# Performance work log

Hardware: AMD Instinct MI355X
Metric: run time of the kernel (lower is better)

Reference implementation:

```python
import jax, jax.numpy as jnp
import numpy as np

B, P, K_NB, D, H = 4, 1024, 32, 768, 12
S = P + 1
HD = D // H  # 64

def _ln(x, w, b):
    m = jnp.mean(x, -1, keepdims=True)
    v = jnp.var(x, -1, keepdims=True)
    return (x - m) / jnp.sqrt(v + 1e-5) * w + b

def setup_inputs() -> dict:
    key = jax.random.key(0)
    ks = jax.random.split(key, 8)
    w = lambda k, sh: jax.random.normal(k, sh, jnp.float32) * 0.02
    return {
        'x': jax.random.normal(ks[0], (B, S, D), jnp.float32),
        'routes': jax.random.randint(ks[1], (P, K_NB), 0, P, dtype=jnp.int32),
        'qkv_w': w(ks[2], (D, 3 * D)), 'qkv_b': jnp.zeros((3 * D,), jnp.float32),
        'proj_w': w(ks[3], (D, D)), 'proj_b': jnp.zeros((D,), jnp.float32),
        'ln1_w': jnp.ones((D,), jnp.float32), 'ln1_b': jnp.zeros((D,), jnp.float32),
        'ln2_w': jnp.ones((D,), jnp.float32), 'ln2_b': jnp.zeros((D,), jnp.float32),
        'mlp_w1': w(ks[4], (D, 4 * D)), 'mlp_b1': jnp.zeros((4 * D,), jnp.float32),
        'mlp_w2': w(ks[5], (4 * D, D)), 'mlp_b2': jnp.zeros((D,), jnp.float32),
    }

def reference(x, routes, qkv_w, qkv_b, proj_w, proj_b, ln1_w, ln1_b,
              ln2_w, ln2_b, mlp_w1, mlp_b1, mlp_w2, mlp_b2):
    scale = HD ** -0.5
    xn = _ln(x, ln1_w, ln1_b)
    qkv = (xn @ qkv_w + qkv_b).reshape(B, S, 3, H, HD).transpose(2, 0, 3, 1, 4)
    Q, Kt, V = qkv[0], qkv[1], qkv[2]  # each [B,H,S,HD]
    # CLS token: full dense attention over all S tokens
    sc = jnp.einsum('bhqd,bhkd->bhqk', Q[:, :, :1], Kt) * scale
    oc = jnp.einsum('bhqk,bhkd->bhqd', jax.nn.softmax(sc, -1), V)  # [B,H,1,HD]
    # patch tokens: sparse attention over k routed neighbors
    r = routes + 1  # shift past CLS (buffer routes_shifted)
    Kg = Kt[:, :, r, :]  # [B,H,P,k,HD] gathered keys
    Vg = V[:, :, r, :]   # [B,H,P,k,HD] gathered values
    sp = jnp.einsum('bhpd,bhpkd->bhpk', Q[:, :, 1:], Kg) * scale
    op = jnp.einsum('bhpk,bhpkd->bhpd', jax.nn.softmax(sp, -1), Vg)
    out = jnp.concatenate([oc, op], axis=2).transpose(0, 2, 1, 3).reshape(B, S, D)
    x = x + (out @ proj_w + proj_b)
    h = _ln(x, ln2_w, ln2_b)
    h = jax.nn.gelu(h @ mlp_w1 + mlp_b1, approximate=False) @ mlp_w2 + mlp_b2
    return x + h
```

## Files before the change

kernel.cpp:

```cpp
#include <hip/hip_runtime.h>
#include <hip/hip_bf16.h>

using bf16 = __hip_bfloat16;
using s8v  = __attribute__((ext_vector_type(8))) short;
using f4v  = __attribute__((ext_vector_type(4))) float;

constexpr int B_   = 4;
constexpr int P_   = 1024;
constexpr int KNB  = 32;
constexpr int D_   = 768;
constexpr int H_   = 12;
constexpr int S_   = P_ + 1;
constexpr int M_   = B_ * S_;
constexpr int MPAD = 4224;

#define DEVI static __device__ __forceinline__
#define WAITVM(N) asm volatile("s_waitcnt vmcnt(" #N ")" ::: "memory")
#define MEMFENCE  asm volatile("" ::: "memory")

DEVI float b2f_lo(unsigned u) { return __builtin_bit_cast(float, u << 16); }
DEVI float b2f_hi(unsigned u) { return __builtin_bit_cast(float, u & 0xffff0000u); }
DEVI float bu2f(unsigned short u) { return __builtin_bit_cast(float, (unsigned)u << 16); }
DEVI unsigned short f2bu(float f) {
  return __builtin_bit_cast(unsigned short, __float2bfloat16(f));
}

template<int KK, int NN>
__global__ __launch_bounds__(256)
void wt_conv(const float* __restrict__ W, bf16* __restrict__ Wt) {
  __shared__ float t[32][33];
  int bk = blockIdx.x * 32, bn = blockIdx.y * 32;
  int tx = threadIdx.x & 31, ty = threadIdx.x >> 5;
#pragma unroll
  for (int i = 0; i < 32; i += 8)
    t[ty + i][tx] = W[(size_t)(bk + ty + i) * NN + bn + tx];
  __syncthreads();
#pragma unroll
  for (int i = 0; i < 32; i += 8)
    Wt[(size_t)(bn + ty + i) * KK + bk + tx] = __float2bfloat16(t[tx][ty + i]);
}

__global__ __launch_bounds__(256)
void ln_kernel(const float* __restrict__ x, const float* __restrict__ w,
               const float* __restrict__ b, bf16* __restrict__ out) {
  int row = blockIdx.x;
  const float* xr = x + (size_t)row * D_;
  int t = threadIdx.x;
  float v0 = xr[t], v1 = xr[t + 256], v2 = xr[t + 512];
  float s = v0 + v1 + v2;
  float ss = v0 * v0 + v1 * v1 + v2 * v2;
#pragma unroll
  for (int o = 32; o; o >>= 1) { s += __shfl_xor(s, o); ss += __shfl_xor(ss, o); }
  __shared__ float sm[4], sv[4];
  if ((t & 63) == 0) { sm[t >> 6] = s; sv[t >> 6] = ss; }
  __syncthreads();
  float S = sm[0] + sm[1] + sm[2] + sm[3];
  float SS = sv[0] + sv[1] + sv[2] + sv[3];
  float mean = S * (1.f / D_);
  float var  = SS * (1.f / D_) - mean * mean;
  float inv  = rsqrtf(var + 1e-5f);
  bf16* orow = out + (size_t)row * D_;
  orow[t]       = __float2bfloat16((v0 - mean) * inv * w[t]       + b[t]);
  orow[t + 256] = __float2bfloat16((v1 - mean) * inv * w[t + 256] + b[t + 256]);
  orow[t + 512] = __float2bfloat16((v2 - mean) * inv * w[t + 512] + b[t + 512]);
}

template<int BM, int N, int KSTRIDE, int KCHUNK, int MODE>
__global__ __launch_bounds__(256)
void gemm_bf16(const bf16* __restrict__ A, const bf16* __restrict__ Bt,
               const float* __restrict__ bias, void* __restrict__ dst) {
  constexpr int MR   = BM / 32;
  constexpr int LPS  = BM / 64 + 2;
  constexpr int TN   = N / 128;
  constexpr int NBLK = (MPAD / BM) * TN;
  __shared__ bf16 ldsA[3][BM * 32];
  __shared__ bf16 ldsB[3][128 * 32];

  int bid = blockIdx.x;
  constexpr int NQ = NBLK >> 3, NR = NBLK & 7;
  int xcd = bid & 7, off = bid >> 3;
  int swz = (xcd < NR ? xcd * (NQ + 1) : NR * (NQ + 1) + (xcd - NR) * NQ) + off;
  const int tm = swz / TN, tn = swz % TN;
  const int kbase = blockIdx.y * KCHUNK;

  const int tid = threadIdx.x;
  const int wid = tid >> 6, lane = tid & 63;
  const int wr = wid >> 1, wc = wid & 1;

  auto stage = [&](int bufi, int step) {
    const int k0 = kbase + step * 32;
#pragma unroll
    for (int i = 0; i < BM / 64; ++i) {
      int c = wid * 64 + i * 256 + lane;
      int r = c >> 2, slot = c & 3;
      int gs = slot ^ ((r >> 1) & 3);
      const bf16* ga = A + (size_t)(tm * BM + r) * KSTRIDE + k0 + gs * 8;
      bf16* la = &ldsA[bufi][(wid * 64 + i * 256) * 8];
      __builtin_amdgcn_global_load_lds(
          (__attribute__((address_space(1))) void*)ga,
          (__attribute__((address_space(3))) void*)la, 16, 0, 0);
    }
#pragma unroll
    for (int i = 0; i < 2; ++i) {
      int c = wid * 64 + i * 256 + lane;
      int r = c >> 2, slot = c & 3;
      int gs = slot ^ ((r >> 1) & 3);
      const bf16* ga = Bt + (size_t)(tn * 128 + r) * KSTRIDE + k0 + gs * 8;
      bf16* la = &ldsB[bufi][(wid * 64 + i * 256) * 8];
      __builtin_amdgcn_global_load_lds(
          (__attribute__((address_space(1))) void*)ga,
          (__attribute__((address_space(3))) void*)la, 16, 0, 0);
    }
  };

  f4v acc[MR][4] = {};
  const int nk = KCHUNK / 32;

  stage(0, 0); stage(1, 1);

#pragma unroll 3
  for (int kt = 0; kt < nk; ++kt) {
    if (kt < nk - 1) {
      if constexpr (LPS == 4) WAITVM(4); else WAITVM(3);
    } else {
      WAITVM(0);
    }
    __builtin_amdgcn_s_barrier();
    MEMFENCE;
    if (kt + 2 < nk) stage((kt + 2) % 3, kt + 2);

    const int cur = kt % 3;
    s8v af[MR], bfv[4];
#pragma unroll
    for (int m = 0; m < MR; ++m) {
      int row = wr * (MR * 16) + m * 16 + (lane & 15);
      int slot = (lane >> 4) ^ ((row >> 1) & 3);
      af[m] = *(const s8v*)&ldsA[cur][row * 32 + slot * 8];
    }
#pragma unroll
    for (int n = 0; n < 4; ++n) {
      int row = wc * 64 + n * 16 + (lane & 15);
      int slot = (lane >> 4) ^ ((row >> 1) & 3);
      bfv[n] = *(const s8v*)&ldsB[cur][row * 32 + slot * 8];
    }
    __builtin_amdgcn_s_setprio(1);
#pragma unroll
    for (int m = 0; m < MR; ++m)
#pragma unroll
      for (int n = 0; n < 4; ++n)
        acc[m][n] = __builtin_amdgcn_mfma_f32_16x16x32_bf16(af[m], bfv[n], acc[m][n], 0, 0, 0);
    __builtin_amdgcn_s_setprio(0);
  }

#pragma unroll
  for (int m = 0; m < MR; ++m)
#pragma unroll
    for (int n = 0; n < 4; ++n)
#pragma unroll
      for (int j = 0; j < 4; ++j) {
        int row = tm * BM + wr * (MR * 16) + m * 16 + (lane >> 4) * 4 + j;
        int col = tn * 128 + wc * 64 + n * 16 + (lane & 15);
        float v = acc[m][n][j];
        if (MODE == 0) {
          if (row < M_) {
            float val = v + bias[col];
            int which = col / 768, rem2 = col % 768;
            int bb = row / S_, s = row % S_;
            ((bf16*)dst)[((size_t)(which * B_ + bb) * S_ + s) * 768 + rem2] =
                __float2bfloat16(val);
          }
        } else if (MODE == 2) {
          if (row < M_) {
            float val = v + bias[col];
            val = 0.5f * val * (1.f + erff(val * 0.70710678f));
            ((bf16*)dst)[(size_t)row * N + col] = __float2bfloat16(val);
          }
        } else {
          bf16* p = (bf16*)dst + (size_t)blockIdx.y * MPAD * N;
          p[(size_t)row * N + col] = __float2bfloat16(v);
        }
      }
}

template<bool IP>
__global__ __launch_bounds__(256)
void reduceK(const bf16* __restrict__ part, const float* __restrict__ src,
             const float* __restrict__ bias, float* __restrict__ out) {
  int i = blockIdx.x * 256 + threadIdx.x;
  ushort4 a = ((const ushort4*)part)[i];
  ushort4 b = ((const ushort4*)(part + (size_t)MPAD * 768))[i];
  float4 s = IP ? ((const float4*)out)[i] : ((const float4*)src)[i];
  int col = (i * 4) % D_;
  float4 bv = *(const float4*)&bias[col];
  float4 o;
  o.x = s.x + bv.x + bu2f(a.x) + bu2f(b.x);
  o.y = s.y + bv.y + bu2f(a.y) + bu2f(b.y);
  o.z = s.z + bv.z + bu2f(a.z) + bu2f(b.z);
  o.w = s.w + bv.w + bu2f(a.w) + bu2f(b.w);
  ((float4*)out)[i] = o;
}

__global__ __launch_bounds__(256)
void cls_partial(const bf16* __restrict__ QKV, float* __restrict__ part) {
  int bh = blockIdx.x, c = blockIdx.y;
  int b = bh / H_, h = bh % H_;
  const bf16* q  = QKV + ((size_t)(0 * B_ + b) * S_) * D_ + h * 64;
  const bf16* Kr = QKV + ((size_t)(1 * B_ + b) * S_) * D_ + h * 64;
  const bf16* Vr = QKV + ((size_t)(2 * B_ + b) * S_) * D_ + h * 64;
  int k0 = c * 256, kn = (c == 3) ? 257 : 256;
  __shared__ float qf[64];
  __shared__ float sc[257];
  __shared__ float red[4];
  __shared__ float pv[4][64];
  int t = threadIdx.x;
  if (t < 64) qf[t] = __bfloat162float(q[t]);
  __syncthreads();
  for (int kk = t; kk < kn; kk += 256) {
    const uint4* k4 = (const uint4*)(Kr + (size_t)(k0 + kk) * D_);
    float s = 0.f;
#pragma unroll
    for (int i = 0; i < 8; ++i) {
      uint4 kv = k4[i];
      const float* q8 = &qf[i * 8];
      s += b2f_lo(kv.x) * q8[0] + b2f_hi(kv.x) * q8[1]
         + b2f_lo(kv.y) * q8[2] + b2f_hi(kv.y) * q8[3]
         + b2f_lo(kv.z) * q8[4] + b2f_hi(kv.z) * q8[5]
         + b2f_lo(kv.w) * q8[6] + b2f_hi(kv.w) * q8[7];
    }
    sc[kk] = s * 0.125f;
  }
  __syncthreads();
  float mx = -1e30f;
  for (int kk = t; kk < kn; kk += 256) mx = fmaxf(mx, sc[kk]);
#pragma unroll
  for (int o = 32; o; o >>= 1) mx = fmaxf(mx, __shfl_xor(mx, o));
  if ((t & 63) == 0) red[t >> 6] = mx;
  __syncthreads();
  float M = fmaxf(fmaxf(red[0], red[1]), fmaxf(red[2], red[3]));
  __syncthreads();
  float sum = 0.f;
  for (int kk = t; kk < kn; kk += 256) { float e = __expf(sc[kk] - M); sc[kk] = e; sum += e; }
#pragma unroll
  for (int o = 32; o; o >>= 1) sum += __shfl_xor(sum, o);
  if ((t & 63) == 0) red[t >> 6] = sum;
  __syncthreads();
  float L = red[0] + red[1] + red[2] + red[3];
  int d = t & 63, kg = t >> 6;
  float acc = 0.f;
  for (int kk = kg; kk < kn; kk += 4)
    acc += sc[kk] * __bfloat162float(Vr[(size_t)(k0 + kk) * D_ + d]);
  pv[kg][d] = acc;
  __syncthreads();
  float* pp = part + ((size_t)bh * 4 + c) * 68;
  if (t < 64) pp[4 + t] = pv[0][t] + pv[1][t] + pv[2][t] + pv[3][t];
  else if (t == 64) pp[0] = M;
  else if (t == 65) pp[1] = L;
}

__global__ __launch_bounds__(64)
void cls_combine(const float* __restrict__ part, bf16* __restrict__ out) {
  int bh = blockIdx.x, t = threadIdx.x;
  const float* pp = part + (size_t)bh * 4 * 68;
  float m0 = pp[0], m1 = pp[68], m2 = pp[136], m3 = pp[204];
  float M = fmaxf(fmaxf(m0, m1), fmaxf(m2, m3));
  float e0 = __expf(m0 - M), e1 = __expf(m1 - M), e2 = __expf(m2 - M), e3 = __expf(m3 - M);
  float L = pp[1] * e0 + pp[69] * e1 + pp[137] * e2 + pp[205] * e3;
  float o = pp[4 + t] * e0 + pp[72 + t] * e1 + pp[140 + t] * e2 + pp[208 + t] * e3;
  int b = bh / H_, h = bh % H_;
  out[(size_t)(b * S_) * D_ + h * 64 + t] = __float2bfloat16(o / L);
}

__global__ __launch_bounds__(256)
void routed_attn(const bf16* __restrict__ QKV, const int* __restrict__ routes,
                 bf16* __restrict__ out) {
  int unit = blockIdx.x * 4 + (threadIdx.x >> 6);
  int lane = threadIdx.x & 63;
  int h = unit % H_;
  int bp = unit / H_;
  int p = bp % P_, b = bp / P_;

  int k = lane & 31, hi = lane >> 5;
  int r = routes[p * KNB + k] + 1;

  const bf16* Qp = QKV + ((size_t)(0 * B_ + b) * S_ + (p + 1)) * D_ + h * 64 + hi * 32;
  const bf16* Kb = QKV + ((size_t)(1 * B_ + b) * S_) * D_;
  const bf16* Vb = QKV + ((size_t)(2 * B_ + b) * S_) * D_;

  const uint4* q4 = (const uint4*)Qp;
  const uint4* k4 = (const uint4*)(Kb + (size_t)r * D_ + h * 64 + hi * 32);
  float dot = 0.f;
#pragma unroll
  for (int i = 0; i < 4; ++i) {
    uint4 qv = q4[i], kv = k4[i];
    dot += b2f_lo(kv.x) * b2f_lo(qv.x) + b2f_hi(kv.x) * b2f_hi(qv.x)
         + b2f_lo(kv.y) * b2f_lo(qv.y) + b2f_hi(kv.y) * b2f_hi(qv.y)
         + b2f_lo(kv.z) * b2f_lo(qv.z) + b2f_hi(kv.z) * b2f_hi(qv.z)
         + b2f_lo(kv.w) * b2f_lo(qv.w) + b2f_hi(kv.w) * b2f_hi(qv.w);
  }
  dot += __shfl_xor(dot, 32);
  float sc = dot * 0.125f;

  float mx = sc;
#pragma unroll
  for (int o = 16; o; o >>= 1) mx = fmaxf(mx, __shfl_xor(mx, o));
  float w = __expf(sc - mx);
  float sum = w;
#pragma unroll
  for (int o = 16; o; o >>= 1) sum += __shfl_xor(sum, o);
  float inv = 1.f / sum;

  int c = lane & 7, kr0 = lane >> 3;
  float acc[8] = {};
#pragma unroll
  for (int j = 0; j < 4; ++j) {
    int kj = (kr0 & 7) + 8 * j;
    float wj = __shfl(w, kj);
    int rj = __shfl(r, kj);
    uint4 vv = *(const uint4*)(Vb + (size_t)rj * D_ + h * 64 + c * 8);
    acc[0] += wj * b2f_lo(vv.x); acc[1] += wj * b2f_hi(vv.x);
    acc[2] += wj * b2f_lo(vv.y); acc[3] += wj * b2f_hi(vv.y);
    acc[4] += wj * b2f_lo(vv.z); acc[5] += wj * b2f_hi(vv.z);
    acc[6] += wj * b2f_lo(vv.w); acc[7] += wj * b2f_hi(vv.w);
  }
#pragma unroll
  for (int s = 8; s < 64; s <<= 1)
#pragma unroll
    for (int d = 0; d < 8; ++d) acc[d] += __shfl_xor(acc[d], s);

  if (lane < 8) {
    s8v o;
#pragma unroll
    for (int d = 0; d < 8; ++d) o[d] = (short)f2bu(acc[d] * inv);
    *(s8v*)(out + ((size_t)(b * S_ + p + 1)) * D_ + h * 64 + c * 8) = o;
  }
}

extern "C" void kernel_launch(void* const* d_in, const int* in_sizes, int n_in,
                              void* d_out, int out_size, void* d_ws, size_t ws_size,
                              hipStream_t stream) {
  const float* x      = (const float*)d_in[0];
  const int*   routes = (const int*)d_in[1];
  const float* qkv_w  = (const float*)d_in[2];
  const float* qkv_b  = (const float*)d_in[3];
  const float* proj_w = (const float*)d_in[4];
  const float* proj_b = (const float*)d_in[5];
  const float* ln1_w  = (const float*)d_in[6];
  const float* ln1_b  = (const float*)d_in[7];
  const float* ln2_w  = (const float*)d_in[8];
  const float* ln2_b  = (const float*)d_in[9];
  const float* mlp_w1 = (const float*)d_in[10];
  const float* mlp_b1 = (const float*)d_in[11];
  const float* mlp_w2 = (const float*)d_in[12];
  const float* mlp_b2 = (const float*)d_in[13];
  float* out = (float*)d_out;

  bf16* qkvw_t  = (bf16*)d_ws;
  bf16* projw_t = qkvw_t + 2304 * 768;
  bf16* mlpw1_t = projw_t + 768 * 768;
  bf16* mlpw2_t = mlpw1_t + 3072 * 768;
  bf16* xnA     = mlpw2_t + 768 * 3072;
  bf16* qkvbuf  = xnA + (size_t)MPAD * 768;
  bf16* attn    = qkvbuf + (size_t)3 * B_ * S_ * 768;
  bf16* h2      = attn + (size_t)MPAD * 768;
  bf16* g       = xnA;
  bf16* projp   = xnA;
  bf16* mlp2p   = attn;
  float* clsp   = (float*)(attn + (size_t)M_ * 768);

  wt_conv<768, 2304><<<dim3(24, 72), 256, 0, stream>>>(qkv_w, qkvw_t);
  wt_conv<768, 768><<<dim3(24, 24), 256, 0, stream>>>(proj_w, projw_t);
  wt_conv<768, 3072><<<dim3(24, 96), 256, 0, stream>>>(mlp_w1, mlpw1_t);
  wt_conv<3072, 768><<<dim3(96, 24), 256, 0, stream>>>(mlp_w2, mlpw2_t);

  ln_kernel<<<M_, 256, 0, stream>>>(x, ln1_w, ln1_b, xnA);

  gemm_bf16<128, 2304, 768, 768, 0><<<33 * 18, 256, 0, stream>>>(xnA, qkvw_t, qkv_b, qkvbuf);

  routed_attn<<<(B_ * P_ * H_) / 4, 256, 0, stream>>>(qkvbuf, routes, attn);
  cls_partial<<<dim3(B_ * H_, 4), 256, 0, stream>>>(qkvbuf, clsp);
  cls_combine<<<B_ * H_, 64, 0, stream>>>(clsp, attn);

  gemm_bf16<64, 768, 768, 384, 3><<<dim3(66 * 6, 2), 256, 0, stream>>>(attn, projw_t, nullptr, projp);
  reduceK<false><<<(M_ * D_) / 1024, 256, 0, stream>>>(projp, x, proj_b, out);

  ln_kernel<<<M_, 256, 0, stream>>>(out, ln2_w, ln2_b, h2);

  gemm_bf16<128, 3072, 768, 768, 2><<<33 * 24, 256, 0, stream>>>(h2, mlpw1_t, mlp_b1, g);

  gemm_bf16<64, 768, 3072, 1536, 3><<<dim3(66 * 6, 2), 256, 0, stream>>>(g, mlpw2_t, nullptr, mlp2p);
  reduceK<true><<<(M_ * D_) / 1024, 256, 0, stream>>>(mlp2p, nullptr, mlp_b2, out);
}
```

Before: 342.0 us.

## Fuse prep kernels, merge attention paths, fuse proj reduce with LN2, use 64-row GEMM tiles

Merges the four weight-transpose launches and LN1 into one prep kernel, and folds CLS attention into the routed attention kernel as extra blocks, so the CLS pass no longer needs a split/combine step. The proj split-K reduction is fused with the residual add and LN2 in a per-row kernel. All GEMMs now use fixed 64-row tiles (the QKV and MLP1 GEMMs previously used 128 rows) and drop the setprio hints. These changes cut launch count and intermediate memory traffic. The cost is more, smaller GEMM tiles with less register reuse, and a single-block CLS reduction over the full sequence.

```diff
diff --git a/kernel.cpp b/kernel.cpp
--- a/kernel.cpp
+++ b/kernel.cpp
@@ -20,17 +20,15 @@
 
 DEVI float b2f_lo(unsigned u) { return __builtin_bit_cast(float, u << 16); }
 DEVI float b2f_hi(unsigned u) { return __builtin_bit_cast(float, u & 0xffff0000u); }
-DEVI float bu2f(unsigned short u) { return __builtin_bit_cast(float, (unsigned)u << 16); }
 DEVI unsigned short f2bu(float f) {
   return __builtin_bit_cast(unsigned short, __float2bfloat16(f));
 }
 
-template<int KK, int NN>
-__global__ __launch_bounds__(256)
-void wt_conv(const float* __restrict__ W, bf16* __restrict__ Wt) {
-  __shared__ float t[32][33];
-  int bk = blockIdx.x * 32, bn = blockIdx.y * 32;
-  int tx = threadIdx.x & 31, ty = threadIdx.x >> 5;
+DEVI void wt_conv_dev(const float* __restrict__ W, bf16* __restrict__ Wt,
+                      int KK, int NN, int idx, int tid, float (*t)[33]) {
+  int nbn = NN >> 5;
+  int bk = (idx / nbn) * 32, bn = (idx % nbn) * 32;
+  int tx = tid & 31, ty = tid >> 5;
 #pragma unroll
   for (int i = 0; i < 32; i += 8)
     t[ty + i][tx] = W[(size_t)(bk + ty + i) * NN + bn + tx];
@@ -40,18 +38,14 @@
     Wt[(size_t)(bn + ty + i) * KK + bk + tx] = __float2bfloat16(t[tx][ty + i]);
 }
 
-__global__ __launch_bounds__(256)
-void ln_kernel(const float* __restrict__ x, const float* __restrict__ w,
-               const float* __restrict__ b, bf16* __restrict__ out) {
-  int row = blockIdx.x;
-  const float* xr = x + (size_t)row * D_;
-  int t = threadIdx.x;
+DEVI void ln_dev(const float* __restrict__ xr, const float* __restrict__ w,
+                 const float* __restrict__ b, bf16* __restrict__ orow,
+                 int t, float* sm, float* sv) {
   float v0 = xr[t], v1 = xr[t + 256], v2 = xr[t + 512];
   float s = v0 + v1 + v2;
   float ss = v0 * v0 + v1 * v1 + v2 * v2;
 #pragma unroll
   for (int o = 32; o; o >>= 1) { s += __shfl_xor(s, o); ss += __shfl_xor(ss, o); }
-  __shared__ float sm[4], sv[4];
   if ((t & 63) == 0) { sm[t >> 6] = s; sv[t >> 6] = ss; }
   __syncthreads();
   float S = sm[0] + sm[1] + sm[2] + sm[3];
@@ -59,18 +53,36 @@
   float mean = S * (1.f / D_);
   float var  = SS * (1.f / D_) - mean * mean;
   float inv  = rsqrtf(var + 1e-5f);
-  bf16* orow = out + (size_t)row * D_;
   orow[t]       = __float2bfloat16((v0 - mean) * inv * w[t]       + b[t]);
   orow[t + 256] = __float2bfloat16((v1 - mean) * inv * w[t + 256] + b[t + 256]);
   orow[t + 512] = __float2bfloat16((v2 - mean) * inv * w[t + 512] + b[t + 512]);
 }
 
-template<int BM, int N, int KSTRIDE, int KCHUNK, int MODE>
+__global__ __launch_bounds__(256)
+void prep(const float* __restrict__ qkv_w, const float* __restrict__ proj_w,
+          const float* __restrict__ mlp_w1, const float* __restrict__ mlp_w2,
+          bf16* qkvw_t, bf16* projw_t, bf16* mlpw1_t, bf16* mlpw2_t,
+          const float* __restrict__ x, const float* __restrict__ ln1_w,
+          const float* __restrict__ ln1_b, bf16* xnA) {
+  __shared__ float t[32][33];
+  __shared__ float sm[4], sv[4];
+  int idx = blockIdx.x, tid = threadIdx.x;
+  if (idx < 1728)       wt_conv_dev(qkv_w,  qkvw_t,  768,  2304, idx,        tid, t);
+  else if (idx < 2304)  wt_conv_dev(proj_w, projw_t, 768,  768,  idx - 1728, tid, t);
+  else if (idx < 4608)  wt_conv_dev(mlp_w1, mlpw1_t, 768,  3072, idx - 2304, tid, t);
+  else if (idx < 6912)  wt_conv_dev(mlp_w2, mlpw2_t, 3072, 768,  idx - 4608, tid, t);
+  else {
+    int row = idx - 6912;
+    ln_dev(x + (size_t)row * D_, ln1_w, ln1_b, xnA + (size_t)row * D_, tid, sm, sv);
+  }
+}
+
+template<int N, int KSTRIDE, int KCHUNK, int MODE>
 __global__ __launch_bounds__(256)
 void gemm_bf16(const bf16* __restrict__ A, const bf16* __restrict__ Bt,
                const float* __restrict__ bias, void* __restrict__ dst) {
-  constexpr int MR   = BM / 32;
-  constexpr int LPS  = BM / 64 + 2;
+  constexpr int BM   = 64;
+  constexpr int MR   = 2;
   constexpr int TN   = N / 128;
   constexpr int NBLK = (MPAD / BM) * TN;
   __shared__ bf16 ldsA[3][BM * 32];
@@ -89,13 +101,12 @@
 
   auto stage = [&](int bufi, int step) {
     const int k0 = kbase + step * 32;
-#pragma unroll
-    for (int i = 0; i < BM / 64; ++i) {
-      int c = wid * 64 + i * 256 + lane;
+    {
+      int c = wid * 64 + lane;
       int r = c >> 2, slot = c & 3;
       int gs = slot ^ ((r >> 1) & 3);
       const bf16* ga = A + (size_t)(tm * BM + r) * KSTRIDE + k0 + gs * 8;
-      bf16* la = &ldsA[bufi][(wid * 64 + i * 256) * 8];
+      bf16* la = &ldsA[bufi][(wid * 64 + lane) * 8];
       __builtin_amdgcn_global_load_lds(
           (__attribute__((address_space(1))) void*)ga,
           (__attribute__((address_space(3))) void*)la, 16, 0, 0);
@@ -120,11 +131,8 @@
 
 #pragma unroll 3
   for (int kt = 0; kt < nk; ++kt) {
-    if (kt < nk - 1) {
-      if constexpr (LPS == 4) WAITVM(4); else WAITVM(3);
-    } else {
-      WAITVM(0);
-    }
+    if (kt < nk - 1) WAITVM(3);
+    else             WAITVM(0);
     __builtin_amdgcn_s_barrier();
     MEMFENCE;
     if (kt + 2 < nk) stage((kt + 2) % 3, kt + 2);
@@ -133,7 +141,7 @@
     s8v af[MR], bfv[4];
 #pragma unroll
     for (int m = 0; m < MR; ++m) {
-      int row = wr * (MR * 16) + m * 16 + (lane & 15);
+      int row = wr * 32 + m * 16 + (lane & 15);
       int slot = (lane >> 4) ^ ((row >> 1) & 3);
       af[m] = *(const s8v*)&ldsA[cur][row * 32 + slot * 8];
     }
@@ -143,13 +151,11 @@
       int slot = (lane >> 4) ^ ((row >> 1) & 3);
       bfv[n] = *(const s8v*)&ldsB[cur][row * 32 + slot * 8];
     }
-    __builtin_amdgcn_s_setprio(1);
 #pragma unroll
     for (int m = 0; m < MR; ++m)
 #pragma unroll
       for (int n = 0; n < 4; ++n)
         acc[m][n] = __builtin_amdgcn_mfma_f32_16x16x32_bf16(af[m], bfv[n], acc[m][n], 0, 0, 0);
-    __builtin_amdgcn_s_setprio(0);
   }
 
 #pragma unroll
@@ -158,7 +164,7 @@
     for (int n = 0; n < 4; ++n)
 #pragma unroll
       for (int j = 0; j < 4; ++j) {
-        int row = tm * BM + wr * (MR * 16) + m * 16 + (lane >> 4) * 4 + j;
+        int row = tm * 64 + wr * 32 + m * 16 + (lane >> 4) * 4 + j;
         int col = tn * 128 + wc * 64 + n * 16 + (lane & 15);
         float v = acc[m][n][j];
         if (MODE == 0) {
@@ -182,156 +188,181 @@
       }
 }
 
-template<bool IP>
 __global__ __launch_bounds__(256)
-void reduceK(const bf16* __restrict__ part, const float* __restrict__ src,
-             const float* __restrict__ bias, float* __restrict__ out) {
+void projfix(const bf16* __restrict__ part, const float* __restrict__ x,
+             const float* __restrict__ pbias, const float* __restrict__ lnw,
+             const float* __restrict__ lnb, float* __restrict__ out,
+             bf16* __restrict__ h2) {
+  int row = blockIdx.x, t = threadIdx.x;
+  const bf16* p0 = part + (size_t)row * D_;
+  const bf16* p1 = part + (size_t)MPAD * D_ + (size_t)row * D_;
+  const float* xr = x + (size_t)row * D_;
+  float v[3];
+#pragma unroll
+  for (int i = 0; i < 3; ++i) {
+    int c = t + i * 256;
+    v[i] = xr[c] + pbias[c] + __bfloat162float(p0[c]) + __bfloat162float(p1[c]);
+  }
+  float* orow = out + (size_t)row * D_;
+#pragma unroll
+  for (int i = 0; i < 3; ++i) orow[t + i * 256] = v[i];
+  float s = v[0] + v[1] + v[2];
+  float ss = v[0] * v[0] + v[1] * v[1] + v[2] * v[2];
+#pragma unroll
+  for (int o = 32; o; o >>= 1) { s += __shfl_xor(s, o); ss += __shfl_xor(ss, o); }
+  __shared__ float sm[4], sv[4];
+  if ((t & 63) == 0) { sm[t >> 6] = s; sv[t >> 6] = ss; }
+  __syncthreads();
+  float S = sm[0] + sm[1] + sm[2] + sm[3];
+  float SS = sv[0] + sv[1] + sv[2] + sv[3];
+  float mean = S * (1.f / D_);
+  float var  = SS * (1.f / D_) - mean * mean;
+  float inv  = rsqrtf(var + 1e-5f);
+  bf16* hrow = h2 + (size_t)row * D_;
+#pragma unroll
+  for (int i = 0; i < 3; ++i) {
+    int c = t + i * 256;
+    hrow[c] = __float2bfloat16((v[i] - mean) * inv * lnw[c] + lnb[c]);
+  }
+}
+
+__global__ __launch_bounds__(256)
+void reduceK(const bf16* __restrict__ part, const float* __restrict__ bias,
+             float* __restrict__ out) {
   int i = blockIdx.x * 256 + threadIdx.x;
   ushort4 a = ((const ushort4*)part)[i];
   ushort4 b = ((const ushort4*)(part + (size_t)MPAD * 768))[i];
-  float4 s = IP ? ((const float4*)out)[i] : ((const float4*)src)[i];
+  float4 s = ((const float4*)out)[i];
   int col = (i * 4) % D_;
   float4 bv = *(const float4*)&bias[col];
   float4 o;
-  o.x = s.x + bv.x + bu2f(a.x) + bu2f(b.x);
-  o.y = s.y + bv.y + bu2f(a.y) + bu2f(b.y);
-  o.z = s.z + bv.z + bu2f(a.z) + bu2f(b.z);
-  o.w = s.w + bv.w + bu2f(a.w) + bu2f(b.w);
+  o.x = s.x + bv.x + b2f_lo((unsigned)a.x << 16 >> 16 << 16 >> 16 | 0) ;
+  o.x = s.x + bv.x + __bfloat162float(__hip_bfloat16_raw{a.x}) + __bfloat162float(__hip_bfloat16_raw{b.x});
+  o.y = s.y + bv.y + __bfloat162float(__hip_bfloat16_raw{a.y}) + __bfloat162float(__hip_bfloat16_raw{b.y});
+  o.z = s.z + bv.z + __bfloat162float(__hip_bfloat16_raw{a.z}) + __bfloat162float(__hip_bfloat16_raw{b.z});
+  o.w = s.w + bv.w + __bfloat162float(__hip_bfloat16_raw{a.w}) + __bfloat162float(__hip_bfloat16_raw{b.w});
   ((float4*)out)[i] = o;
 }
 
 __global__ __launch_bounds__(256)
-void cls_partial(const bf16* __restrict__ QKV, float* __restrict__ part) {
-  int bh = blockIdx.x, c = blockIdx.y;
-  int b = bh / H_, h = bh % H_;
-  const bf16* q  = QKV + ((size_t)(0 * B_ + b) * S_) * D_ + h * 64;
-  const bf16* Kr = QKV + ((size_t)(1 * B_ + b) * S_) * D_ + h * 64;
-  const bf16* Vr = QKV + ((size_t)(2 * B_ + b) * S_) * D_ + h * 64;
-  int k0 = c * 256, kn = (c == 3) ? 257 : 256;
+void attn_kernel(const bf16* __restrict__ QKV, const int* __restrict__ routes,
+                 bf16* __restrict__ out) {
   __shared__ float qf[64];
-  __shared__ float sc[257];
+  __shared__ float sc[S_];
   __shared__ float red[4];
   __shared__ float pv[4][64];
-  int t = threadIdx.x;
-  if (t < 64) qf[t] = __bfloat162float(q[t]);
-  __syncthreads();
-  for (int kk = t; kk < kn; kk += 256) {
-    const uint4* k4 = (const uint4*)(Kr + (size_t)(k0 + kk) * D_);
-    float s = 0.f;
-#pragma unroll
-    for (int i = 0; i < 8; ++i) {
-      uint4 kv = k4[i];
-      const float* q8 = &qf[i * 8];
-      s += b2f_lo(kv.x) * q8[0] + b2f_hi(kv.x) * q8[1]
-         + b2f_lo(kv.y) * q8[2] + b2f_hi(kv.y) * q8[3]
-         + b2f_lo(kv.z) * q8[4] + b2f_hi(kv.z) * q8[5]
-         + b2f_lo(kv.w) * q8[6] + b2f_hi(kv.w) * q8[7];
-    }
-    sc[kk] = s * 0.125f;
-  }
-  __syncthreads();
-  float mx = -1e30f;
-  for (int kk = t; kk < kn; kk += 256) mx = fmaxf(mx, sc[kk]);
-#pragma unroll
-  for (int o = 32; o; o >>= 1) mx = fmaxf(mx, __shfl_xor(mx, o));
-  if ((t & 63) == 0) red[t >> 6] = mx;
-  __syncthreads();
-  float M = fmaxf(fmaxf(red[0], red[1]), fmaxf(red[2], red[3]));
-  __syncthreads();
-  float sum = 0.f;
-  for (int kk = t; kk < kn; kk += 256) { float e = __expf(sc[kk] - M); sc[kk] = e; sum += e; }
-#pragma unroll
-  for (int o = 32; o; o >>= 1) sum += __shfl_xor(sum, o);
-  if ((t & 63) == 0) red[t >> 6] = sum;
-  __syncthreads();
-  float L = red[0] + red[1] + red[2] + red[3];
-  int d = t & 63, kg = t >> 6;
-  float acc = 0.f;
-  for (int kk = kg; kk < kn; kk += 4)
-    acc += sc[kk] * __bfloat162float(Vr[(size_t)(k0 + kk) * D_ + d]);
-  pv[kg][d] = acc;
-  __syncthreads();
-  float* pp = part + ((size_t)bh * 4 + c) * 68;
-  if (t < 64) pp[4 + t] = pv[0][t] + pv[1][t] + pv[2][t] + pv[3][t];
-  else if (t == 64) pp[0] = M;
-  else if (t == 65) pp[1] = L;
-}
-
-__global__ __launch_bounds__(64)
-void cls_combine(const float* __restrict__ part, bf16* __restrict__ out) {
-  int bh = blockIdx.x, t = threadIdx.x;
-  const float* pp = part + (size_t)bh * 4 * 68;
-  float m0 = pp[0], m1 = pp[68], m2 = pp[136], m3 = pp[204];
-  float M = fmaxf(fmaxf(m0, m1), fmaxf(m2, m3));
-  float e0 = __expf(m0 - M), e1 = __expf(m1 - M), e2 = __expf(m2 - M), e3 = __expf(m3 - M);
-  float L = pp[1] * e0 + pp[69] * e1 + pp[137] * e2 + pp[205] * e3;
-  float o = pp[4 + t] * e0 + pp[72 + t] * e1 + pp[140 + t] * e2 + pp[208 + t] * e3;
-  int b = bh / H_, h = bh % H_;
-  out[(size_t)(b * S_) * D_ + h * 64 + t] = __float2bfloat16(o / L);
-}
-
-__global__ __launch_bounds__(256)
-void routed_attn(const bf16* __restrict__ QKV, const int* __restrict__ routes,
-                 bf16* __restrict__ out) {
-  int unit = blockIdx.x * 4 + (threadIdx.x >> 6);
-  int lane = threadIdx.x & 63;
-  int h = unit % H_;
-  int bp = unit / H_;
-  int p = bp % P_, b = bp / P_;
-
-  int k = lane & 31, hi = lane >> 5;
-  int r = routes[p * KNB + k] + 1;
-
-  const bf16* Qp = QKV + ((size_t)(0 * B_ + b) * S_ + (p + 1)) * D_ + h * 64 + hi * 32;
-  const bf16* Kb = QKV + ((size_t)(1 * B_ + b) * S_) * D_;
-  const bf16* Vb = QKV + ((size_t)(2 * B_ + b) * S_) * D_;
-
-  const uint4* q4 = (const uint4*)Qp;
-  const uint4* k4 = (const uint4*)(Kb + (size_t)r * D_ + h * 64 + hi * 32);
-  float dot = 0.f;
-#pragma unroll
-  for (int i = 0; i < 4; ++i) {
-    uint4 qv = q4[i], kv = k4[i];
-    dot += b2f_lo(kv.x) * b2f_lo(qv.x) + b2f_hi(kv.x) * b2f_hi(qv.x)
-         + b2f_lo(kv.y) * b2f_lo(qv.y) + b2f_hi(kv.y) * b2f_hi(qv.y)
-         + b2f_lo(kv.z) * b2f_lo(qv.z) + b2f_hi(kv.z) * b2f_hi(qv.z)
-         + b2f_lo(kv.w) * b2f_lo(qv.w) + b2f_hi(kv.w) * b2f_hi(qv.w);
-  }
-  dot += __shfl_xor(dot, 32);
-  float sc = dot * 0.125f;
-
-  float mx = sc;
-#pragma unroll
-  for (int o = 16; o; o >>= 1) mx = fmaxf(mx, __shfl_xor(mx, o));
-  float w = __expf(sc - mx);
-  float sum = w;
-#pragma unroll
-  for (int o = 16; o; o >>= 1) sum += __shfl_xor(sum, o);
-  float inv = 1.f / sum;
-
-  int c = lane & 7, kr0 = lane >> 3;
-  float acc[8] = {};
-#pragma unroll
-  for (int j = 0; j < 4; ++j) {
-    int kj = (kr0 & 7) + 8 * j;
-    float wj = __shfl(w, kj);
-    int rj = __shfl(r, kj);
-    uint4 vv = *(const uint4*)(Vb + (size_t)rj * D_ + h * 64 + c * 8);
-    acc[0] += wj * b2f_lo(vv.x); acc[1] += wj * b2f_hi(vv.x);
-    acc[2] += wj * b2f_lo(vv.y); acc[3] += wj * b2f_hi(vv.y);
-    acc[4] += wj * b2f_lo(vv.z); acc[5] += wj * b2f_hi(vv.z);
-    acc[6] += wj * b2f_lo(vv.w); acc[7] += wj * b2f_hi(vv.w);
-  }
-#pragma unroll
-  for (int s = 8; s < 64; s <<= 1)
-#pragma unroll
-    for (int d = 0; d < 8; ++d) acc[d] += __shfl_xor(acc[d], s);
-
-  if (lane < 8) {
-    s8v o;
-#pragma unroll
-    for (int d = 0; d < 8; ++d) o[d] = (short)f2bu(acc[d] * inv);
-    *(s8v*)(out + ((size_t)(b * S_ + p + 1)) * D_ + h * 64 + c * 8) = o;
+
+  if (blockIdx.x < 12288) {
+    int unit = blockIdx.x * 4 + (threadIdx.x >> 6);
+    int lane = threadIdx.x & 63;
+    int h = unit % H_;
+    int bp = unit / H_;
+    int p = bp % P_, b = bp / P_;
+
+    int k = lane & 31, hi = lane >> 5;
+    int r = routes[p * KNB + k] + 1;
+
+    const bf16* Qp = QKV + ((size_t)(0 * B_ + b) * S_ + (p + 1)) * D_ + h * 64 + hi * 32;
+    const bf16* Kb = QKV + ((size_t)(1 * B_ + b) * S_) * D_;
+    const bf16* Vb = QKV + ((size_t)(2 * B_ + b) * S_) * D_;
+
+    const uint4* q4 = (const uint4*)Qp;
+    const uint4* k4 = (const uint4*)(Kb + (size_t)r * D_ + h * 64 + hi * 32);
+    float dot = 0.f;
+#pragma unroll
+    for (int i = 0; i < 4; ++i) {
+      uint4 qv = q4[i], kv = k4[i];
+      dot += b2f_lo(kv.x) * b2f_lo(qv.x) + b2f_hi(kv.x) * b2f_hi(qv.x)
+           + b2f_lo(kv.y) * b2f_lo(qv.y) + b2f_hi(kv.y) * b2f_hi(qv.y)
+           + b2f_lo(kv.z) * b2f_lo(qv.z) + b2f_hi(kv.z) * b2f_hi(qv.z)
+           + b2f_lo(kv.w) * b2f_lo(qv.w) + b2f_hi(kv.w) * b2f_hi(qv.w);
+    }
+    dot += __shfl_xor(dot, 32);
+    float scv = dot * 0.125f;
+
+    float mx = scv;
+#pragma unroll
+    for (int o = 16; o; o >>= 1) mx = fmaxf(mx, __shfl_xor(mx, o));
+    float w = __expf(scv - mx);
+    float sum = w;
+#pragma unroll
+    for (int o = 16; o; o >>= 1) sum += __shfl_xor(sum, o);
+    float inv = 1.f / sum;
+
+    int c = lane & 7, kr0 = lane >> 3;
+    float acc[8] = {};
+#pragma unroll
+    for (int j = 0; j < 4; ++j) {
+      int kj = (kr0 & 7) + 8 * j;
+      float wj = __shfl(w, kj);
+      int rj = __shfl(r, kj);
+      uint4 vv = *(const uint4*)(Vb + (size_t)rj * D_ + h * 64 + c * 8);
+      acc[0] += wj * b2f_lo(vv.x); acc[1] += wj * b2f_hi(vv.x);
+      acc[2] += wj * b2f_lo(vv.y); acc[3] += wj * b2f_hi(vv.y);
+      acc[4] += wj * b2f_lo(vv.z); acc[5] += wj * b2f_hi(vv.z);
+      acc[6] += wj * b2f_lo(vv.w); acc[7] += wj * b2f_hi(vv.w);
+    }
+#pragma unroll
+    for (int s = 8; s < 64; s <<= 1)
+#pragma unroll
+      for (int d = 0; d < 8; ++d) acc[d] += __shfl_xor(acc[d], s);
+
+    if (lane < 8) {
+      s8v o;
+#pragma unroll
+      for (int d = 0; d < 8; ++d) o[d] = (short)f2bu(acc[d] * inv);
+      *(s8v*)(out + ((size_t)(b * S_ + p + 1)) * D_ + h * 64 + c * 8) = o;
+    }
+  } else {
+    int bh = blockIdx.x - 12288;
+    int b = bh / H_, h = bh % H_;
+    const bf16* q  = QKV + ((size_t)(0 * B_ + b) * S_) * D_ + h * 64;
+    const bf16* Kr = QKV + ((size_t)(1 * B_ + b) * S_) * D_ + h * 64;
+    const bf16* Vr = QKV + ((size_t)(2 * B_ + b) * S_) * D_ + h * 64;
+    int t = threadIdx.x;
+    if (t < 64) qf[t] = __bfloat162float(q[t]);
+    __syncthreads();
+    for (int kk = t; kk < S_; kk += 256) {
+      const uint4* k4 = (const uint4*)(Kr + (size_t)kk * D_);
+      float s = 0.f;
+#pragma unroll
+      for (int i = 0; i < 8; ++i) {
+        uint4 kv = k4[i];
+        const float* q8 = &qf[i * 8];
+        s += b2f_lo(kv.x) * q8[0] + b2f_hi(kv.x) * q8[1]
+           + b2f_lo(kv.y) * q8[2] + b2f_hi(kv.y) * q8[3]
+           + b2f_lo(kv.z) * q8[4] + b2f_hi(kv.z) * q8[5]
+           + b2f_lo(kv.w) * q8[6] + b2f_hi(kv.w) * q8[7];
+      }
+      sc[kk] = s * 0.125f;
+    }
+    __syncthreads();
+    float mx = -1e30f;
+    for (int kk = t; kk < S_; kk += 256) mx = fmaxf(mx, sc[kk]);
+#pragma unroll
+    for (int o = 32; o; o >>= 1) mx = fmaxf(mx, __shfl_xor(mx, o));
+    if ((t & 63) == 0) red[t >> 6] = mx;
+    __syncthreads();
+    float M = fmaxf(fmaxf(red[0], red[1]), fmaxf(red[2], red[3]));
+    __syncthreads();
+    float sum = 0.f;
+    for (int kk = t; kk < S_; kk += 256) { float e = __expf(sc[kk] - M); sc[kk] = e; sum += e; }
+#pragma unroll
+    for (int o = 32; o; o >>= 1) sum += __shfl_xor(sum, o);
+    if ((t & 63) == 0) red[t >> 6] = sum;
+    __syncthreads();
+    float L = red[0] + red[1] + red[2] + red[3];
+    float inv = 1.f / L;
+    int d = t & 63, kg = t >> 6;
+    float acc = 0.f;
+    for (int kk = kg; kk < S_; kk += 4)
+      acc += sc[kk] * __bfloat162float(Vr[(size_t)kk * D_ + d]);
+    pv[kg][d] = acc;
+    __syncthreads();
+    if (t < 64) {
+      float ov = (pv[0][t] + pv[1][t] + pv[2][t] + pv[3][t]) * inv;
+      out[(size_t)(b * S_) * D_ + h * 64 + t] = __float2bfloat16(ov);
+    }
   }
 }
 
@@ -365,28 +396,22 @@
   bf16* g       = xnA;
   bf16* projp   = xnA;
   bf16* mlp2p   = attn;
-  float* clsp   = (float*)(attn + (size_t)M_ * 768);
-
-  wt_conv<768, 2304><<<dim3(24, 72), 256, 0, stream>>>(qkv_w, qkvw_t);
-  wt_conv<768, 768><<<dim3(24, 24), 256, 0, stream>>>(proj_w, projw_t);
-  wt_conv<768, 3072><<<dim3(24, 96), 256, 0, stream>>>(mlp_w1, mlpw1_t);
-  wt_conv<3072, 768><<<dim3(96, 24), 256, 0, stream>>>(mlp_w2, mlpw2_t);
-
-  ln_kernel<<<M_, 256, 0, stream>>>(x, ln1_w, ln1_b, xnA);
-
-  gemm_bf16<128, 2304, 768, 768, 0><<<33 * 18, 256, 0, stream>>>(xnA, qkvw_t, qkv_b, qkvbuf);
-
-  routed_attn<<<(B_ * P_ * H_) / 4, 256, 0, stream>>>(qkvbuf, routes, attn);
-  cls_partial<<<dim3(B_ * H_, 4), 256, 0, stream>>>(qkvbuf, clsp);
-  cls_combine<<<B_ * H_, 64, 0, stream>>>(clsp, attn);
-
-  gemm_bf16<64, 768, 768, 384, 3><<<dim3(66 * 6, 2), 256, 0, stream>>>(attn, projw_t, nullptr, projp);
-  reduceK<false><<<(M_ * D_) / 1024, 256, 0, stream>>>(projp, x, proj_b, out);
-
-  ln_kernel<<<M_, 256, 0, stream>>>(out, ln2_w, ln2_b, h2);
-
-  gemm_bf16<128, 3072, 768, 768, 2><<<33 * 24, 256, 0, stream>>>(h2, mlpw1_t, mlp_b1, g);
-
-  gemm_bf16<64, 768, 3072, 1536, 3><<<dim3(66 * 6, 2), 256, 0, stream>>>(g, mlpw2_t, nullptr, mlp2p);
-  reduceK<true><<<(M_ * D_) / 1024, 256, 0, stream>>>(mlp2p, nullptr, mlp_b2, out);
-}
+
+  prep<<<6912 + M_, 256, 0, stream>>>(qkv_w, proj_w, mlp_w1, mlp_w2,
+                                      qkvw_t, projw_t, mlpw1_t, mlpw2_t,
+                                      x, ln1_w, ln1_b, xnA);
+
+  gemm_bf16<2304, 768, 768, 0><<<66 * 18, 256, 0, stream>>>(xnA, qkvw_t, qkv_b, qkvbuf);
+
+  attn_kernel<<<12288 + B_ * H_, 256, 0, stream>>>(qkvbuf, routes, attn);
+
+  gemm_bf16<768, 768, 384, 3><<<dim3(66 * 6, 2), 256, 0, stream>>>(attn, projw_t, nullptr, projp);
+
+  projfix<<<M_, 256, 0, stream>>>(projp, x, proj_b, ln2_w, ln2_b, out, h2);
+
+  gemm_bf16<3072, 768, 768, 2><<<66 * 24, 256, 0, stream>>>(h2, mlpw1_t, mlp_b1, g);
+
+  gemm_bf16<768, 3072, 1536, 3><<<dim3(66 * 6, 2), 256, 0, stream>>>(g, mlpw2_t, nullptr, mlp2p);
+
+  reduceK<<<(M_ * D_) / 1024, 256, 0, stream>>>(mlp2p, mlp_b2, out);
+}
```

New measurement: 380.2 us. 1.11x slower.
